# Kernel optimization log

Hardware: AMD Instinct MI355X
Metric: run time of the kernel (lower is better)

The kernel has to match this reference:

```python
import jax, jax.numpy as jnp
import numpy as np

NEG_INF = -1e20


def setup_inputs() -> dict:
    key = jax.random.key(0)
    kq, kk, kv, kl = jax.random.split(key, 4)
    B, NQ, NKV, D_QK, D_V = 16, 2048, 2048, 64, 64
    Q_batch = jax.random.normal(kq, (B, NQ, D_QK), dtype=jnp.float32)
    K_batch = jax.random.normal(kk, (B, NKV, D_QK), dtype=jnp.float32)
    V_batch = jax.random.normal(kv, (B, NKV, D_V), dtype=jnp.float32)
    valid_lens = jax.random.randint(kl, (B,), 0, NKV, dtype=jnp.int32)
    return {"Q_batch": Q_batch, "K_batch": K_batch, "V_batch": V_batch,
            "valid_lens": valid_lens}


def reference(Q_batch, K_batch, V_batch, valid_lens):
    d = Q_batch.shape[-1]
    # scores: (B, n_q, n_kv)
    S = jnp.einsum("bqd,bkd->bqk", Q_batch, K_batch) / jnp.sqrt(
        jnp.asarray(d, dtype=Q_batch.dtype))
    n_kv = S.shape[-1]
    # mask kv positions k >= valid_lens[b] (1-D valid_lens broadcast over queries)
    kv_idx = jnp.arange(n_kv)  # (n_kv,)
    mask = kv_idx[None, None, :] < valid_lens[:, None, None]  # (B,1,n_kv)
    S = jnp.where(mask, S, NEG_INF)
    W = jax.nn.softmax(S, axis=-1)
    # dropout rate is 0.0 (eval) -> identity
    return jnp.einsum("bqk,bkv->bqv", W, V_batch)
```

## Files before the change

kernel.cpp:

```cpp
#include <hip/hip_runtime.h>
#include <hip/hip_bf16.h>


typedef __attribute__((ext_vector_type(8))) short short8;
typedef __attribute__((ext_vector_type(4))) short short4v;
typedef __attribute__((ext_vector_type(4))) float float4v;
typedef __attribute__((ext_vector_type(16))) float f32x16;

#define BATCH 16
#define NQ 2048
#define NKV 2048
#define DH 64
#define KVB 64
#define NTILES (NKV / KVB)
#define TILE_ELEMS (KVB * DH)
#define NEG_INF -1e20f
#define SCALE_LOG2 0.180336880111120f

__device__ __forceinline__ short f2bf(float x) {
    union { float f; unsigned u; } v; v.f = x;
    unsigned r = (v.u + 0x7fffu + ((v.u >> 16) & 1u)) >> 16;
    return (short)r;
}

__device__ __forceinline__ short8 cvt8(float4v a, float4v b) {
    short8 r;
    r[0] = f2bf(a[0]); r[1] = f2bf(a[1]); r[2] = f2bf(a[2]); r[3] = f2bf(a[3]);
    r[4] = f2bf(b[0]); r[5] = f2bf(b[1]); r[6] = f2bf(b[2]); r[7] = f2bf(b[3]);
    return r;
}

__device__ __forceinline__ float fexp2(float x) {
    float r; asm("v_exp_f32 %0, %1" : "=v"(r) : "v"(x)); return r;
}

__global__ __launch_bounds__(256) void prep_kernel(
    const float* __restrict__ K, const float* __restrict__ V,
    const int* __restrict__ valid_lens,
    short* __restrict__ Kf, short* __restrict__ Vf)
{
    const int b    = blockIdx.x >> 5;
    const int tile = blockIdx.x & 31;
    const int vlen = valid_lens[b];
    const int nkv  = (vlen == 0) ? NKV : vlen;
    if (tile * KVB >= nkv) return;

    const int tid = threadIdx.x;
    const int ln  = tid & 63;
    const int l31 = ln & 31;
    const int hi8 = (ln >> 5) * 8;
    const size_t gbase = ((size_t)b * NKV + (size_t)tile * KVB) * DH;
    short* kt = Kf + (((size_t)b * NTILES + tile) * TILE_ELEMS);
    short* vt = Vf + (((size_t)b * NTILES + tile) * TILE_ELEMS);

#pragma unroll
    for (int s = 0; s < 2; ++s) {
        const int kk = tid >> 6;
        const int kv = s * 32 + l31;
        const int d  = kk * 16 + hi8;
        const float* p = K + gbase + (size_t)kv * DH + d;
        *reinterpret_cast<short8*>(kt + (s * 256 + tid) * 8) =
            cvt8(*reinterpret_cast<const float4v*>(p),
                 *reinterpret_cast<const float4v*>(p + 4));
    }
    {
        const int kv0 = (tid >> 4) << 2;
        const int d0  = (tid & 15) << 2;
        const float* p = V + gbase + (size_t)kv0 * DH + d0;
        float4v r0 = *reinterpret_cast<const float4v*>(p);
        float4v r1 = *reinterpret_cast<const float4v*>(p + DH);
        float4v r2 = *reinterpret_cast<const float4v*>(p + 2 * DH);
        float4v r3 = *reinterpret_cast<const float4v*>(p + 3 * DH);
        const int ks  = kv0 >> 4;
        const int hiv = (kv0 >> 3) & 1;
        const int j0  = kv0 & 7;
#pragma unroll
        for (int k = 0; k < 4; ++k) {
            const int d    = d0 + k;
            const int lanev = (d & 31) + 32 * hiv;
            short4v w;
            w[0] = f2bf(r0[k]); w[1] = f2bf(r1[k]);
            w[2] = f2bf(r2[k]); w[3] = f2bf(r3[k]);
            *reinterpret_cast<short4v*>(
                vt + (((d >> 5) * 4 + ks) * 64 + lanev) * 8 + j0) = w;
        }
    }
}

__global__ __launch_bounds__(512) void attn_fwd_kernel(
    const float* __restrict__ Q,
    const short* __restrict__ Kf,
    const short* __restrict__ Vf,
    const int* __restrict__ vl,
    float* __restrict__ O)
{
    __shared__ float  mrg[2][4][32][68];
    __shared__ float2 mlb[2][4][32];

    const int tid  = threadIdx.x;
    const int wave = tid >> 6;
    const int lane = tid & 63;
    const int l31  = lane & 31;
    const int hi   = lane >> 5;
    const int qsub = wave >> 2;
    const int kvq  = wave & 3;

    const int x      = blockIdx.x & 7;
    const int parity = blockIdx.x >> 8;
    const int qt     = (blockIdx.x >> 3) & 31;
    const int wrank  = parity ? (15 - x) : x;

    int tv;
    {
        const int v  = vl[lane & 15];
        const int nk = (v == 0) ? NKV : v;
        tv = (nk + KVB - 1) >> 6;
    }
    int rank = 0;
#pragma unroll
    for (int j = 0; j < 16; ++j) {
        const int tj = __shfl(tv, j, 64);
        rank += (tj > tv) || (tj == tv && j < (lane & 15));
    }
    const unsigned long long mk = __ballot((lane < 16) && (rank == wrank));
    const int b = __ffsll(mk) - 1;

    const int vlen  = vl[b];
    const int nkv   = (vlen == 0) ? NKV : vlen;
    const int tiles = (nkv + KVB - 1) >> 6;
    const int nh    = (tiles - kvq + 3) >> 2;
    const int qbase = qt * 64 + qsub * 32;

    const float* Qb = Q + ((size_t)b * NQ + qbase + l31) * DH;
    short8 qfrag[4];
#pragma unroll
    for (int kk = 0; kk < 4; ++kk) {
        const float* p = Qb + kk * 16 + hi * 8;
        float4v a = *reinterpret_cast<const float4v*>(p);
        float4v c = *reinterpret_cast<const float4v*>(p + 4);
#pragma unroll
        for (int j = 0; j < 4; ++j) { a[j] *= SCALE_LOG2; c[j] *= SCALE_LOG2; }
        qfrag[kk] = cvt8(a, c);
    }

    const short* Kfb = Kf + (size_t)b * NTILES * TILE_ELEMS + lane * 8;
    const short* Vfb = Vf + (size_t)b * NTILES * TILE_ELEMS + lane * 8;

    auto load_k = [&](short8 (&kf)[8], int tile) {
        const short* p = Kfb + (size_t)tile * TILE_ELEMS;
#pragma unroll
        for (int i = 0; i < 8; ++i)
            kf[i] = *reinterpret_cast<const short8*>(p + i * 512);
    };

    f32x16 acc_oA[2], acc_oB[2];
#pragma unroll
    for (int t = 0; t < 2; ++t)
#pragma unroll
        for (int r = 0; r < 16; ++r) { acc_oA[t][r] = 0.f; acc_oB[t][r] = 0.f; }
    float m = -INFINITY, lsum = 0.f;

    short8 kf0[8], kf1[8];

    auto body = [&](short8 (&kc)[8], short8 (&kn)[8], f32x16 (&am)[2], int it) {
        const int tile = 4 * it + kvq;

        short8 vfr[8];
        {
            const short* p = Vfb + (size_t)tile * TILE_ELEMS;
#pragma unroll
            for (int i = 0; i < 8; ++i)
                vfr[i] = *reinterpret_cast<const short8*>(p + i * 512);
        }

        f32x16 acs[2];
#pragma unroll
        for (int s = 0; s < 2; ++s)
#pragma unroll
            for (int r = 0; r < 16; ++r) acs[s][r] = 0.f;
        __builtin_amdgcn_s_setprio(1);
#pragma unroll
        for (int s = 0; s < 2; ++s)
#pragma unroll
            for (int kk = 0; kk < 4; ++kk)
                acs[s] = __builtin_amdgcn_mfma_f32_32x32x16_bf16(
                    kc[s * 4 + kk], qfrag[kk], acs[s], 0, 0, 0);
        __builtin_amdgcn_s_setprio(0);

        if (it + 1 < nh) load_k(kn, 4 * (it + 1) + kvq);

        if (vlen < (tile + 1) * KVB) {
            const int kvb0 = tile * KVB + 4 * hi;
#pragma unroll
            for (int s = 0; s < 2; ++s) {
                const int vlim = vlen - (kvb0 + s * 32);
#pragma unroll
                for (int r = 0; r < 16; ++r) {
                    const int rc = (r & 3) + 8 * (r >> 2);
                    acs[s][r] = (rc < vlim) ? acs[s][r] : NEG_INF;
                }
            }
        }

        float mx[8];
#pragma unroll
        for (int r = 0; r < 8; ++r)
            mx[r] = fmaxf(fmaxf(acs[0][r], acs[0][r + 8]),
                          fmaxf(acs[1][r], acs[1][r + 8]));
#pragma unroll
        for (int d = 4; d; d >>= 1)
#pragma unroll
            for (int r = 0; r < d; ++r) mx[r] = fmaxf(mx[r], mx[r + d]);
        float xv = mx[0];
        xv = fmaxf(xv, __shfl_xor(xv, 32, 64));

        float mn = m;
        if (!__all(xv <= m + 8.f)) {
            mn = fmaxf(m, xv);
            const float alpha = fexp2(m - mn);
            m = mn;
            lsum *= alpha;
#pragma unroll
            for (int r = 0; r < 16; ++r) {
                const int rc = (r & 3) + 8 * (r >> 2);
                const float ar = __shfl(alpha, rc + 4 * hi, 64);
                acc_oA[0][r] *= ar; acc_oA[1][r] *= ar;
                acc_oB[0][r] *= ar; acc_oB[1][r] *= ar;
            }
        }

#pragma unroll
        for (int s = 0; s < 2; ++s)
#pragma unroll
            for (int r = 0; r < 16; ++r) acs[s][r] = fexp2(acs[s][r] - mn);
        float sm[8];
#pragma unroll
        for (int r = 0; r < 8; ++r)
            sm[r] = (acs[0][r] + acs[0][r + 8]) + (acs[1][r] + acs[1][r + 8]);
#pragma unroll
        for (int d = 4; d; d >>= 1)
#pragma unroll
            for (int r = 0; r < d; ++r) sm[r] += sm[r + d];
        float rs = sm[0];
        rs += __shfl_xor(rs, 32, 64);
        lsum += rs;

        unsigned pk[2][4][2];
#pragma unroll
        for (int s = 0; s < 2; ++s)
#pragma unroll
            for (int be = 0; be < 4; ++be)
#pragma unroll
                for (int c = 0; c < 2; ++c)
                    asm("v_cvt_pk_bf16_f32 %0, %1, %2"
                        : "=v"(pk[s][be][c])
                        : "v"(acs[s][4 * be + 2 * c]),
                          "v"(acs[s][4 * be + 2 * c + 1]));

        __builtin_amdgcn_s_setprio(1);
#pragma unroll
        for (int ks = 0; ks < 4; ++ks) {
            const int s = ks >> 1, g = ks & 1;
            unsigned w0 = pk[s][2 * g][0], w2 = pk[s][2 * g + 1][0];
            unsigned w1 = pk[s][2 * g][1], w3 = pk[s][2 * g + 1][1];
            asm("v_permlane32_swap_b32 %0, %1" : "+v"(w0), "+v"(w2));
            asm("v_permlane32_swap_b32 %0, %1" : "+v"(w1), "+v"(w3));
            union { unsigned u[4]; short8 s8; } pf;
            pf.u[0] = w0; pf.u[1] = w1; pf.u[2] = w2; pf.u[3] = w3;
#pragma unroll
            for (int t = 0; t < 2; ++t)
                am[t] = __builtin_amdgcn_mfma_f32_32x32x16_bf16(
                    pf.s8, vfr[t * 4 + ks], am[t], 0, 0, 0);
        }
        __builtin_amdgcn_s_setprio(0);
    };

    if (nh > 0) load_k(kf0, kvq);
    int it = 0;
    for (; it + 1 < nh; it += 2) {
        body(kf0, kf1, acc_oA, it);
        body(kf1, kf0, acc_oB, it + 1);
    }
    if (it < nh) body(kf0, kf1, acc_oA, it);

#pragma unroll
    for (int t = 0; t < 2; ++t)
#pragma unroll
        for (int r = 0; r < 16; ++r) acc_oA[t][r] += acc_oB[t][r];

#pragma unroll
    for (int t = 0; t < 2; ++t)
#pragma unroll
        for (int r = 0; r < 16; ++r) {
            const int rc = (r & 3) + 8 * (r >> 2);
            mrg[qsub][kvq][rc + 4 * hi][t * 32 + l31] = acc_oA[t][r];
        }
    if (lane < 32) mlb[qsub][kvq][l31] = float2{m, lsum};
    __syncthreads();

    {
        const int qsubo = wave >> 2;
        const int qq = (wave & 3) * 8 + (lane >> 3);
        const int dg = (lane & 7) * 8;
        float mi[4], li[4];
#pragma unroll
        for (int ii = 0; ii < 4; ++ii) {
            const float2 c = mlb[qsubo][ii][qq];
            mi[ii] = c.x; li[ii] = c.y;
        }
        const float M = fmaxf(fmaxf(mi[0], mi[1]), fmaxf(mi[2], mi[3]));
        float wgt[4], L = 0.f;
#pragma unroll
        for (int ii = 0; ii < 4; ++ii) {
            wgt[ii] = fexp2(mi[ii] - M);
            L += li[ii] * wgt[ii];
        }
        const float Linv = 1.f / L;
#pragma unroll
        for (int ii = 0; ii < 4; ++ii) wgt[ii] *= Linv;

        float4v o0 = {0.f, 0.f, 0.f, 0.f}, o1 = {0.f, 0.f, 0.f, 0.f};
#pragma unroll
        for (int ii = 0; ii < 4; ++ii) {
            const float* src = &mrg[qsubo][ii][qq][dg];
            float4v a = *reinterpret_cast<const float4v*>(src);
            float4v c = *reinterpret_cast<const float4v*>(src + 4);
#pragma unroll
            for (int j = 0; j < 4; ++j) {
                o0[j] += a[j] * wgt[ii]; o1[j] += c[j] * wgt[ii];
            }
        }
        float* Ob = O + ((size_t)b * NQ + qt * 64 + qsubo * 32 + qq) * DH + dg;
        *reinterpret_cast<float4v*>(Ob)     = o0;
        *reinterpret_cast<float4v*>(Ob + 4) = o1;
    }
}

extern "C" void kernel_launch(void* const* d_in, const int* in_sizes, int n_in,
                              void* d_out, int out_size, void* d_ws, size_t ws_size,
                              hipStream_t stream) {
    const float* Q = (const float*)d_in[0];
    const float* K = (const float*)d_in[1];
    const float* V = (const float*)d_in[2];
    const int* vl  = (const int*)d_in[3];
    float* Out     = (float*)d_out;

    short* Kws = (short*)d_ws;
    short* Vws = Kws + (size_t)BATCH * NTILES * TILE_ELEMS;

    prep_kernel<<<dim3(BATCH * NTILES), dim3(256), 0, stream>>>(K, V, vl, Kws, Vws);
    attn_fwd_kernel<<<dim3(512), dim3(512), 0, stream>>>(Q, Kws, Vws, vl, Out);
}
```

Before: 35.27 us.

## Process two 32-row query groups per wave to reuse K/V tile loads

Each wave now handles 64 query rows (two qfrag groups) against each loaded K/V tile, halving the grid to 256 blocks and halving global K/V traffic per query. The load-balancing batch ranking by valid length is dropped in favour of a simple blockIdx mapping, and the double-buffered K prefetch with split accumulators is replaced by a single buffer. Waves-per-EU is pinned at 2 to give more registers for the doubled accumulators. The trade-off is fewer blocks (256 on a large GPU) and the loss of length-aware scheduling, which can leave CUs underused or imbalanced given the random valid lengths.

```diff
diff --git a/kernel.cpp b/kernel.cpp
--- a/kernel.cpp
+++ b/kernel.cpp
@@ -16,6 +16,7 @@
 #define TILE_ELEMS (KVB * DH)
 #define NEG_INF -1e20f
 #define SCALE_LOG2 0.180336880111120f
+#define MPAD 66
 
 __device__ __forceinline__ short f2bf(float x) {
     union { float f; unsigned u; } v; v.f = x;
@@ -87,15 +88,17 @@
     }
 }
 
-__global__ __launch_bounds__(512) void attn_fwd_kernel(
+__global__
+__attribute__((amdgpu_flat_work_group_size(512, 512), amdgpu_waves_per_eu(2, 2)))
+void attn_fwd_kernel(
     const float* __restrict__ Q,
     const short* __restrict__ Kf,
     const short* __restrict__ Vf,
     const int* __restrict__ vl,
     float* __restrict__ O)
 {
-    __shared__ float  mrg[2][4][32][68];
-    __shared__ float2 mlb[2][4][32];
+    __shared__ float  mrg[2][4][64][MPAD];
+    __shared__ float2 mlb[2][4][64];
 
     const int tid  = threadIdx.x;
     const int wave = tid >> 6;
@@ -105,64 +108,54 @@
     const int qsub = wave >> 2;
     const int kvq  = wave & 3;
 
-    const int x      = blockIdx.x & 7;
-    const int parity = blockIdx.x >> 8;
-    const int qt     = (blockIdx.x >> 3) & 31;
-    const int wrank  = parity ? (15 - x) : x;
-
-    int tv;
-    {
-        const int v  = vl[lane & 15];
-        const int nk = (v == 0) ? NKV : v;
-        tv = (nk + KVB - 1) >> 6;
-    }
-    int rank = 0;
-#pragma unroll
-    for (int j = 0; j < 16; ++j) {
-        const int tj = __shfl(tv, j, 64);
-        rank += (tj > tv) || (tj == tv && j < (lane & 15));
-    }
-    const unsigned long long mk = __ballot((lane < 16) && (rank == wrank));
-    const int b = __ffsll(mk) - 1;
+    const int b  = blockIdx.x & 15;
+    const int qt = blockIdx.x >> 4;
+    const int qbase = qt * 128 + qsub * 64;
 
     const int vlen  = vl[b];
     const int nkv   = (vlen == 0) ? NKV : vlen;
     const int tiles = (nkv + KVB - 1) >> 6;
     const int nh    = (tiles - kvq + 3) >> 2;
-    const int qbase = qt * 64 + qsub * 32;
-
-    const float* Qb = Q + ((size_t)b * NQ + qbase + l31) * DH;
-    short8 qfrag[4];
-#pragma unroll
-    for (int kk = 0; kk < 4; ++kk) {
-        const float* p = Qb + kk * 16 + hi * 8;
-        float4v a = *reinterpret_cast<const float4v*>(p);
-        float4v c = *reinterpret_cast<const float4v*>(p + 4);
-#pragma unroll
-        for (int j = 0; j < 4; ++j) { a[j] *= SCALE_LOG2; c[j] *= SCALE_LOG2; }
-        qfrag[kk] = cvt8(a, c);
+
+    short8 qfrag[2][4];
+#pragma unroll
+    for (int qg = 0; qg < 2; ++qg) {
+        const float* Qb = Q + ((size_t)b * NQ + qbase + qg * 32 + l31) * DH;
+#pragma unroll
+        for (int kk = 0; kk < 4; ++kk) {
+            const float* p = Qb + kk * 16 + hi * 8;
+            float4v a = *reinterpret_cast<const float4v*>(p);
+            float4v c = *reinterpret_cast<const float4v*>(p + 4);
+#pragma unroll
+            for (int j = 0; j < 4; ++j) { a[j] *= SCALE_LOG2; c[j] *= SCALE_LOG2; }
+            qfrag[qg][kk] = cvt8(a, c);
+        }
     }
 
     const short* Kfb = Kf + (size_t)b * NTILES * TILE_ELEMS + lane * 8;
     const short* Vfb = Vf + (size_t)b * NTILES * TILE_ELEMS + lane * 8;
 
-    auto load_k = [&](short8 (&kf)[8], int tile) {
+    short8 kf[8];
+    auto load_k = [&](int tile) {
         const short* p = Kfb + (size_t)tile * TILE_ELEMS;
 #pragma unroll
         for (int i = 0; i < 8; ++i)
             kf[i] = *reinterpret_cast<const short8*>(p + i * 512);
     };
 
-    f32x16 acc_oA[2], acc_oB[2];
-#pragma unroll
-    for (int t = 0; t < 2; ++t)
-#pragma unroll
-        for (int r = 0; r < 16; ++r) { acc_oA[t][r] = 0.f; acc_oB[t][r] = 0.f; }
-    float m = -INFINITY, lsum = 0.f;
-
-    short8 kf0[8], kf1[8];
-
-    auto body = [&](short8 (&kc)[8], short8 (&kn)[8], f32x16 (&am)[2], int it) {
+    f32x16 acc[2][2];
+#pragma unroll
+    for (int qg = 0; qg < 2; ++qg)
+#pragma unroll
+        for (int t = 0; t < 2; ++t)
+#pragma unroll
+            for (int r = 0; r < 16; ++r) acc[qg][t][r] = 0.f;
+    float m[2]    = {-INFINITY, -INFINITY};
+    float lsum[2] = {0.f, 0.f};
+
+    if (nh > 0) load_k(kvq);
+
+    for (int it = 0; it < nh; ++it) {
         const int tile = 4 * it + kvq;
 
         short8 vfr[8];
@@ -173,135 +166,138 @@
                 vfr[i] = *reinterpret_cast<const short8*>(p + i * 512);
         }
 
-        f32x16 acs[2];
-#pragma unroll
-        for (int s = 0; s < 2; ++s)
-#pragma unroll
-            for (int r = 0; r < 16; ++r) acs[s][r] = 0.f;
+        f32x16 acs[2][2];
+#pragma unroll
+        for (int qg = 0; qg < 2; ++qg)
+#pragma unroll
+            for (int s = 0; s < 2; ++s)
+#pragma unroll
+                for (int r = 0; r < 16; ++r) acs[qg][s][r] = 0.f;
         __builtin_amdgcn_s_setprio(1);
 #pragma unroll
-        for (int s = 0; s < 2; ++s)
-#pragma unroll
-            for (int kk = 0; kk < 4; ++kk)
-                acs[s] = __builtin_amdgcn_mfma_f32_32x32x16_bf16(
-                    kc[s * 4 + kk], qfrag[kk], acs[s], 0, 0, 0);
+        for (int qg = 0; qg < 2; ++qg)
+#pragma unroll
+            for (int s = 0; s < 2; ++s)
+#pragma unroll
+                for (int kk = 0; kk < 4; ++kk)
+                    acs[qg][s] = __builtin_amdgcn_mfma_f32_32x32x16_bf16(
+                        kf[s * 4 + kk], qfrag[qg][kk], acs[qg][s], 0, 0, 0);
         __builtin_amdgcn_s_setprio(0);
 
-        if (it + 1 < nh) load_k(kn, 4 * (it + 1) + kvq);
+        if (it + 1 < nh) load_k(4 * (it + 1) + kvq);
 
         if (vlen < (tile + 1) * KVB) {
             const int kvb0 = tile * KVB + 4 * hi;
 #pragma unroll
-            for (int s = 0; s < 2; ++s) {
-                const int vlim = vlen - (kvb0 + s * 32);
+            for (int qg = 0; qg < 2; ++qg)
+#pragma unroll
+                for (int s = 0; s < 2; ++s) {
+                    const int vlim = vlen - (kvb0 + s * 32);
+#pragma unroll
+                    for (int r = 0; r < 16; ++r) {
+                        const int rc = (r & 3) + 8 * (r >> 2);
+                        acs[qg][s][r] = (rc < vlim) ? acs[qg][s][r] : NEG_INF;
+                    }
+                }
+        }
+
+#pragma unroll
+        for (int qg = 0; qg < 2; ++qg) {
+            float mx[8];
+#pragma unroll
+            for (int r = 0; r < 8; ++r)
+                mx[r] = fmaxf(fmaxf(acs[qg][0][r], acs[qg][0][r + 8]),
+                              fmaxf(acs[qg][1][r], acs[qg][1][r + 8]));
+#pragma unroll
+            for (int d = 4; d; d >>= 1)
+#pragma unroll
+                for (int r = 0; r < d; ++r) mx[r] = fmaxf(mx[r], mx[r + d]);
+            float xv = mx[0];
+            xv = fmaxf(xv, __shfl_xor(xv, 32, 64));
+
+            float mn = m[qg];
+            if (!__all(xv <= m[qg] + 8.f)) {
+                mn = fmaxf(m[qg], xv);
+                const float alpha = fexp2(m[qg] - mn);
+                m[qg] = mn;
+                lsum[qg] *= alpha;
 #pragma unroll
                 for (int r = 0; r < 16; ++r) {
                     const int rc = (r & 3) + 8 * (r >> 2);
-                    acs[s][r] = (rc < vlim) ? acs[s][r] : NEG_INF;
+                    const float ar = __shfl(alpha, rc + 4 * hi, 64);
+                    acc[qg][0][r] *= ar; acc[qg][1][r] *= ar;
                 }
             }
-        }
-
-        float mx[8];
-#pragma unroll
-        for (int r = 0; r < 8; ++r)
-            mx[r] = fmaxf(fmaxf(acs[0][r], acs[0][r + 8]),
-                          fmaxf(acs[1][r], acs[1][r + 8]));
-#pragma unroll
-        for (int d = 4; d; d >>= 1)
-#pragma unroll
-            for (int r = 0; r < d; ++r) mx[r] = fmaxf(mx[r], mx[r + d]);
-        float xv = mx[0];
-        xv = fmaxf(xv, __shfl_xor(xv, 32, 64));
-
-        float mn = m;
-        if (!__all(xv <= m + 8.f)) {
-            mn = fmaxf(m, xv);
-            const float alpha = fexp2(m - mn);
-            m = mn;
-            lsum *= alpha;
+
+#pragma unroll
+            for (int s = 0; s < 2; ++s)
+#pragma unroll
+                for (int r = 0; r < 16; ++r)
+                    acs[qg][s][r] = fexp2(acs[qg][s][r] - mn);
+            float sm[8];
+#pragma unroll
+            for (int r = 0; r < 8; ++r)
+                sm[r] = (acs[qg][0][r] + acs[qg][0][r + 8]) +
+                        (acs[qg][1][r] + acs[qg][1][r + 8]);
+#pragma unroll
+            for (int d = 4; d; d >>= 1)
+#pragma unroll
+                for (int r = 0; r < d; ++r) sm[r] += sm[r + d];
+            float rs = sm[0];
+            rs += __shfl_xor(rs, 32, 64);
+            lsum[qg] += rs;
+
+            unsigned pk[2][4][2];
+#pragma unroll
+            for (int s = 0; s < 2; ++s)
+#pragma unroll
+                for (int be = 0; be < 4; ++be)
+#pragma unroll
+                    for (int c = 0; c < 2; ++c)
+                        asm("v_cvt_pk_bf16_f32 %0, %1, %2"
+                            : "=v"(pk[s][be][c])
+                            : "v"(acs[qg][s][4 * be + 2 * c]),
+                              "v"(acs[qg][s][4 * be + 2 * c + 1]));
+
+            __builtin_amdgcn_s_setprio(1);
+#pragma unroll
+            for (int ks = 0; ks < 4; ++ks) {
+                const int s = ks >> 1, g = ks & 1;
+                unsigned w0 = pk[s][2 * g][0], w2 = pk[s][2 * g + 1][0];
+                unsigned w1 = pk[s][2 * g][1], w3 = pk[s][2 * g + 1][1];
+                asm("v_permlane32_swap_b32 %0, %1" : "+v"(w0), "+v"(w2));
+                asm("v_permlane32_swap_b32 %0, %1" : "+v"(w1), "+v"(w3));
+                union { unsigned u[4]; short8 s8; } pf;
+                pf.u[0] = w0; pf.u[1] = w1; pf.u[2] = w2; pf.u[3] = w3;
+#pragma unroll
+                for (int t = 0; t < 2; ++t)
+                    acc[qg][t] = __builtin_amdgcn_mfma_f32_32x32x16_bf16(
+                        pf.s8, vfr[t * 4 + ks], acc[qg][t], 0, 0, 0);
+            }
+            __builtin_amdgcn_s_setprio(0);
+        }
+    }
+
+#pragma unroll
+    for (int qg = 0; qg < 2; ++qg)
+#pragma unroll
+        for (int t = 0; t < 2; ++t)
 #pragma unroll
             for (int r = 0; r < 16; ++r) {
                 const int rc = (r & 3) + 8 * (r >> 2);
-                const float ar = __shfl(alpha, rc + 4 * hi, 64);
-                acc_oA[0][r] *= ar; acc_oA[1][r] *= ar;
-                acc_oB[0][r] *= ar; acc_oB[1][r] *= ar;
+                mrg[qsub][kvq][qg * 32 + rc + 4 * hi][t * 32 + l31] =
+                    acc[qg][t][r];
             }
-        }
-
-#pragma unroll
-        for (int s = 0; s < 2; ++s)
-#pragma unroll
-            for (int r = 0; r < 16; ++r) acs[s][r] = fexp2(acs[s][r] - mn);
-        float sm[8];
-#pragma unroll
-        for (int r = 0; r < 8; ++r)
-            sm[r] = (acs[0][r] + acs[0][r + 8]) + (acs[1][r] + acs[1][r + 8]);
-#pragma unroll
-        for (int d = 4; d; d >>= 1)
-#pragma unroll
-            for (int r = 0; r < d; ++r) sm[r] += sm[r + d];
-        float rs = sm[0];
-        rs += __shfl_xor(rs, 32, 64);
-        lsum += rs;
-
-        unsigned pk[2][4][2];
-#pragma unroll
-        for (int s = 0; s < 2; ++s)
-#pragma unroll
-            for (int be = 0; be < 4; ++be)
-#pragma unroll
-                for (int c = 0; c < 2; ++c)
-                    asm("v_cvt_pk_bf16_f32 %0, %1, %2"
-                        : "=v"(pk[s][be][c])
-                        : "v"(acs[s][4 * be + 2 * c]),
-                          "v"(acs[s][4 * be + 2 * c + 1]));
-
-        __builtin_amdgcn_s_setprio(1);
-#pragma unroll
-        for (int ks = 0; ks < 4; ++ks) {
-            const int s = ks >> 1, g = ks & 1;
-            unsigned w0 = pk[s][2 * g][0], w2 = pk[s][2 * g + 1][0];
-            unsigned w1 = pk[s][2 * g][1], w3 = pk[s][2 * g + 1][1];
-            asm("v_permlane32_swap_b32 %0, %1" : "+v"(w0), "+v"(w2));
-            asm("v_permlane32_swap_b32 %0, %1" : "+v"(w1), "+v"(w3));
-            union { unsigned u[4]; short8 s8; } pf;
-            pf.u[0] = w0; pf.u[1] = w1; pf.u[2] = w2; pf.u[3] = w3;
-#pragma unroll
-            for (int t = 0; t < 2; ++t)
-                am[t] = __builtin_amdgcn_mfma_f32_32x32x16_bf16(
-                    pf.s8, vfr[t * 4 + ks], am[t], 0, 0, 0);
-        }
-        __builtin_amdgcn_s_setprio(0);
-    };
-
-    if (nh > 0) load_k(kf0, kvq);
-    int it = 0;
-    for (; it + 1 < nh; it += 2) {
-        body(kf0, kf1, acc_oA, it);
-        body(kf1, kf0, acc_oB, it + 1);
-    }
-    if (it < nh) body(kf0, kf1, acc_oA, it);
-
-#pragma unroll
-    for (int t = 0; t < 2; ++t)
-#pragma unroll
-        for (int r = 0; r < 16; ++r) acc_oA[t][r] += acc_oB[t][r];
-
-#pragma unroll
-    for (int t = 0; t < 2; ++t)
-#pragma unroll
-        for (int r = 0; r < 16; ++r) {
-            const int rc = (r & 3) + 8 * (r >> 2);
-            mrg[qsub][kvq][rc + 4 * hi][t * 32 + l31] = acc_oA[t][r];
-        }
-    if (lane < 32) mlb[qsub][kvq][l31] = float2{m, lsum};
+    if (hi == 0) {
+        mlb[qsub][kvq][l31]      = float2{m[0], lsum[0]};
+        mlb[qsub][kvq][32 + l31] = float2{m[1], lsum[1]};
+    }
     __syncthreads();
 
     {
         const int qsubo = wave >> 2;
-        const int qq = (wave & 3) * 8 + (lane >> 3);
-        const int dg = (lane & 7) * 8;
+        const int qq = (wave & 3) * 16 + (lane >> 2);
+        const int dg = (lane & 3) * 16;
         float mi[4], li[4];
 #pragma unroll
         for (int ii = 0; ii < 4; ++ii) {
@@ -319,20 +315,23 @@
 #pragma unroll
         for (int ii = 0; ii < 4; ++ii) wgt[ii] *= Linv;
 
-        float4v o0 = {0.f, 0.f, 0.f, 0.f}, o1 = {0.f, 0.f, 0.f, 0.f};
+        float4v o[4];
+#pragma unroll
+        for (int j = 0; j < 4; ++j) o[j] = float4v{0.f, 0.f, 0.f, 0.f};
 #pragma unroll
         for (int ii = 0; ii < 4; ++ii) {
             const float* src = &mrg[qsubo][ii][qq][dg];
-            float4v a = *reinterpret_cast<const float4v*>(src);
-            float4v c = *reinterpret_cast<const float4v*>(src + 4);
 #pragma unroll
             for (int j = 0; j < 4; ++j) {
-                o0[j] += a[j] * wgt[ii]; o1[j] += c[j] * wgt[ii];
+                float4v a = *reinterpret_cast<const float4v*>(src + 4 * j);
+#pragma unroll
+                for (int k = 0; k < 4; ++k) o[j][k] += a[k] * wgt[ii];
             }
         }
-        float* Ob = O + ((size_t)b * NQ + qt * 64 + qsubo * 32 + qq) * DH + dg;
-        *reinterpret_cast<float4v*>(Ob)     = o0;
-        *reinterpret_cast<float4v*>(Ob + 4) = o1;
+        float* Ob = O + ((size_t)b * NQ + qt * 128 + qsubo * 64 + qq) * DH + dg;
+#pragma unroll
+        for (int j = 0; j < 4; ++j)
+            *reinterpret_cast<float4v*>(Ob + 4 * j) = o[j];
     }
 }
 
@@ -349,5 +348,5 @@
     short* Vws = Kws + (size_t)BATCH * NTILES * TILE_ELEMS;
 
     prep_kernel<<<dim3(BATCH * NTILES), dim3(256), 0, stream>>>(K, V, vl, Kws, Vws);
-    attn_fwd_kernel<<<dim3(512), dim3(512), 0, stream>>>(Q, Kws, Vws, vl, Out);
-}
+    attn_fwd_kernel<<<dim3(256), dim3(512), 0, stream>>>(Q, Kws, Vws, vl, Out);
+}
```

Result: slower. 42.91 us (+21.7%).
